# Performance work log

Hardware: AMD Instinct MI355X
Metric: run time of the kernel (lower is better)

Reference implementation:

```python
import jax, jax.numpy as jnp
import numpy as np

N_NODES = 100000
N_EDGES = 3200000
F_IN, F_HID, F_OUT = 1433, 8, 7
K = 2  # kernel_size, dim=1, degree-1 B-spline -> basis (1-u, u)
LEAKY_SLOPE = 0.2


def att_spline_conv(x, edge_index, pseudo, w, root, att, bias, n_nodes):
    """Attention SplineConv layer (dim=1, kernel_size=2, linear B-spline).

    w:    [K, in, out] spline kernel weights
    root: [in, out]    root/self weight
    att:  [2*out]      attention vector (src-message part || dst part)
    """
    src, dst = edge_index[0], edge_index[1]
    u = pseudo[:, 0]                                   # [E], in [0,1]
    basis = jnp.stack([1.0 - u, u], axis=1)            # [E, K]
    # transform at node level first (cheap), then gather per edge
    xw = jnp.einsum('ni,kio->nko', x, w)               # [N, K, out]
    m = jnp.einsum('ek,eko->eo', basis, xw[src])       # [E, out] spline message
    h = x @ root                                       # [N, out] root transform
    out_dim = w.shape[-1]
    # GAT-style attention: leaky_relu(a_src . m_e + a_dst . h_dst)
    score = m @ att[:out_dim] + (h @ att[out_dim:])[dst]   # [E]
    score = jax.nn.leaky_relu(score, LEAKY_SLOPE)
    smax = jax.ops.segment_max(score, dst, num_segments=n_nodes)
    e = jnp.exp(score - smax[dst])
    denom = jax.ops.segment_sum(e, dst, num_segments=n_nodes)
    alpha = e / (denom[dst] + 1e-16)                   # segment softmax over dst
    agg = jax.ops.segment_sum(alpha[:, None] * m, dst, num_segments=n_nodes)
    return agg + h + bias


def setup_inputs() -> dict:
    key = jax.random.key(0)
    ks = jax.random.split(key, 12)
    x = jax.random.normal(ks[0], (N_NODES, F_IN), dtype=jnp.float32)
    edge_index = jax.random.randint(ks[1], (2, N_EDGES), 0, N_NODES, dtype=jnp.int64)
    pseudo = jax.random.uniform(ks[2], (N_EDGES, 1), dtype=jnp.float32)
    s1 = 1.0 / np.sqrt(F_IN)
    s2 = 1.0 / np.sqrt(F_HID)
    return {
        'x': x,
        'edge_index': edge_index,
        'pseudo': pseudo,
        'w1': jax.random.normal(ks[3], (K, F_IN, F_HID), dtype=jnp.float32) * s1,
        'root1': jax.random.normal(ks[4], (F_IN, F_HID), dtype=jnp.float32) * s1,
        'att1': jax.random.normal(ks[5], (2 * F_HID,), dtype=jnp.float32) * s2,
        'bias1': jnp.zeros((F_HID,), dtype=jnp.float32),
        'w2': jax.random.normal(ks[6], (K, F_HID, F_OUT), dtype=jnp.float32) * s2,
        'root2': jax.random.normal(ks[7], (F_HID, F_OUT), dtype=jnp.float32) * s2,
        'att2': jax.random.normal(ks[8], (2 * F_OUT,), dtype=jnp.float32) * s2,
        'bias2': jnp.zeros((F_OUT,), dtype=jnp.float32),
    }


def reference(x, edge_index, pseudo, w1, root1, att1, bias1, w2, root2, att2, bias2):
    # eval mode: F.dropout with training=False is identity
    n = x.shape[0]
    h = jax.nn.elu(att_spline_conv(x, edge_index, pseudo, w1, root1, att1, bias1, n))
    h = att_spline_conv(h, edge_index, pseudo, w2, root2, att2, bias2, n)
    return jax.nn.log_softmax(h, axis=1)
```

## Files before the change

### kernel.cpp

```cpp
#include <hip/hip_runtime.h>
#include <math.h>

#define TPB 256
#define F_IN 1433
#define KPAD 1440
#define NT 45
#define NFULL 44
#define ROWS 128

typedef __attribute__((ext_vector_type(8))) short bf16x8;
typedef __attribute__((ext_vector_type(4))) float f32x4;

static __device__ __forceinline__ short f2bf(float f) {
    unsigned u = __float_as_uint(f);
    unsigned r = (u + 0x7FFFu + ((u >> 16) & 1u)) >> 16;
    return (short)r;
}

__global__ __launch_bounds__(256) void prep_kernel(
    const float* __restrict__ w1, const float* __restrict__ root1,
    short* __restrict__ WT, int* __restrict__ cnt, int N)
{
    int i = blockIdx.x * 256 + threadIdx.x;
    if (i < N) cnt[i] = 0;
    if (i < 32 * KPAD) {
        int col = i / KPAD, k = i - col * KPAD;
        float v = 0.f;
        if (k < F_IN) {
            if (col < 8)       v = w1[(size_t)k * 8 + col];
            else if (col < 16) v = w1[(size_t)(F_IN + k) * 8 + (col - 8)];
            else if (col < 24) v = root1[(size_t)k * 8 + (col - 16)];
        }
        WT[i] = f2bf(v);
    }
}

__global__ __launch_bounds__(256) void node1_hist_kernel(
    const float* __restrict__ x,
    const short* __restrict__ WT,
    const float* __restrict__ att1,
    float* __restrict__ XW1,
    float* __restrict__ H1,
    float2* __restrict__ SC1,
    float* __restrict__ HA1,
    const int* __restrict__ ei,
    int* __restrict__ cnt,
    int N, int E, int NB1)
{
    __shared__ float xb[4][32][32];

    const int tid = threadIdx.x;
    const int bid = blockIdx.x;

    if (bid >= NB1) {
        int e = (bid - NB1) * TPB + tid;
        if (e < E) atomicAdd(&cnt[ei[(size_t)E + e]], 1);
        return;
    }

    const int wv   = tid >> 6;
    const int lane = tid & 63;
    const int rowbase = bid * ROWS;

    const int srow   = lane & 7;
    const int schunk = lane >> 3;
    const int pchunk = schunk ^ srow;
    const float* gsrc[4];
#pragma unroll
    for (int g = 0; g < 4; ++g) {
        int r = rowbase + wv * 32 + g * 8 + srow;
        if (r >= N) r = N - 1;
        gsrc[g] = x + (size_t)r * F_IN + schunk * 4;
    }

    const int r0 = lane & 15, r1 = r0 + 16;
    const int klane = (lane >> 4) * 8;
    const int c0 = klane >> 2;
    const int p0 = c0 ^ (r0 & 7);
    const int p1 = (c0 + 1) ^ (r0 & 7);
    const short* wt0 = WT + (size_t)(lane & 15) * KPAD + klane;
    const short* wt1 = wt0 + 16 * KPAD;

    f32x4 acc[2][2];
#pragma unroll
    for (int i = 0; i < 2; ++i)
#pragma unroll
        for (int j = 0; j < 2; ++j)
#pragma unroll
            for (int r = 0; r < 4; ++r) acc[i][j][r] = 0.f;

    {
        float4 V[4];
#pragma unroll
        for (int g = 0; g < 4; ++g) V[g] = *reinterpret_cast<const float4*>(gsrc[g]);
#pragma unroll
        for (int g = 0; g < 4; ++g)
            *reinterpret_cast<float4*>(&xb[wv][g * 8 + srow][pchunk * 4]) = V[g];
    }

    for (int t = 0; t < NFULL; ++t) {
        float4 Vn[4];
        const bool more = (t + 1 < NFULL);
        if (more) {
#pragma unroll
            for (int g = 0; g < 4; ++g)
                Vn[g] = *reinterpret_cast<const float4*>(gsrc[g] + (t + 1) * 32);
        }
        bf16x8 b0 = *reinterpret_cast<const bf16x8*>(wt0 + t * 32);
        bf16x8 b1 = *reinterpret_cast<const bf16x8*>(wt1 + t * 32);
        float4 fa0 = *reinterpret_cast<const float4*>(&xb[wv][r0][p0 * 4]);
        float4 fb0 = *reinterpret_cast<const float4*>(&xb[wv][r0][p1 * 4]);
        float4 fa1 = *reinterpret_cast<const float4*>(&xb[wv][r1][p0 * 4]);
        float4 fb1 = *reinterpret_cast<const float4*>(&xb[wv][r1][p1 * 4]);
        bf16x8 pa0, pa1;
        pa0[0] = f2bf(fa0.x); pa0[1] = f2bf(fa0.y); pa0[2] = f2bf(fa0.z); pa0[3] = f2bf(fa0.w);
        pa0[4] = f2bf(fb0.x); pa0[5] = f2bf(fb0.y); pa0[6] = f2bf(fb0.z); pa0[7] = f2bf(fb0.w);
        pa1[0] = f2bf(fa1.x); pa1[1] = f2bf(fa1.y); pa1[2] = f2bf(fa1.z); pa1[3] = f2bf(fa1.w);
        pa1[4] = f2bf(fb1.x); pa1[5] = f2bf(fb1.y); pa1[6] = f2bf(fb1.z); pa1[7] = f2bf(fb1.w);
        acc[0][0] = __builtin_amdgcn_mfma_f32_16x16x32_bf16(pa0, b0, acc[0][0], 0, 0, 0);
        acc[0][1] = __builtin_amdgcn_mfma_f32_16x16x32_bf16(pa0, b1, acc[0][1], 0, 0, 0);
        acc[1][0] = __builtin_amdgcn_mfma_f32_16x16x32_bf16(pa1, b0, acc[1][0], 0, 0, 0);
        acc[1][1] = __builtin_amdgcn_mfma_f32_16x16x32_bf16(pa1, b1, acc[1][1], 0, 0, 0);
        if (more) {
#pragma unroll
            for (int g = 0; g < 4; ++g)
                *reinterpret_cast<float4*>(&xb[wv][g * 8 + srow][pchunk * 4]) = Vn[g];
        }
    }

    {
        int rr0 = rowbase + wv * 32 + r0; if (rr0 >= N) rr0 = N - 1;
        int rr1 = rowbase + wv * 32 + r1; if (rr1 >= N) rr1 = N - 1;
        const float* xr0 = x + (size_t)rr0 * F_IN;
        const float* xr1 = x + (size_t)rr1 * F_IN;
        const int kf = NFULL * 32 + klane;
        bf16x8 pa0, pa1;
#pragma unroll
        for (int q = 0; q < 8; ++q) {
            float v0 = (kf + q < F_IN) ? xr0[kf + q] : 0.f;
            float v1 = (kf + q < F_IN) ? xr1[kf + q] : 0.f;
            pa0[q] = f2bf(v0);
            pa1[q] = f2bf(v1);
        }
        bf16x8 b0 = *reinterpret_cast<const bf16x8*>(wt0 + NFULL * 32);
        bf16x8 b1 = *reinterpret_cast<const bf16x8*>(wt1 + NFULL * 32);
        acc[0][0] = __builtin_amdgcn_mfma_f32_16x16x32_bf16(pa0, b0, acc[0][0], 0, 0, 0);
        acc[0][1] = __builtin_amdgcn_mfma_f32_16x16x32_bf16(pa0, b1, acc[0][1], 0, 0, 0);
        acc[1][0] = __builtin_amdgcn_mfma_f32_16x16x32_bf16(pa1, b0, acc[1][0], 0, 0, 0);
        acc[1][1] = __builtin_amdgcn_mfma_f32_16x16x32_bf16(pa1, b1, acc[1][1], 0, 0, 0);
    }

    __syncthreads();

    float* dump = reinterpret_cast<float*>(xb);
#pragma unroll
    for (int rt = 0; rt < 2; ++rt)
#pragma unroll
        for (int ot = 0; ot < 2; ++ot) {
            int col = ot * 16 + (lane & 15);
            if (col < 24) {
#pragma unroll
                for (int r = 0; r < 4; ++r) {
                    int row = wv * 32 + rt * 16 + (lane >> 4) * 4 + r;
                    dump[row * 25 + col] = acc[rt][ot][r];
                }
            }
        }
    __syncthreads();

    if (tid < ROWS) {
        int n = rowbase + tid;
        if (n < N) {
            float sum[24];
#pragma unroll
            for (int j = 0; j < 24; ++j) sum[j] = dump[tid * 25 + j];
            float s0 = 0.f, s1 = 0.f, ha = 0.f;
#pragma unroll
            for (int j = 0; j < 8; ++j) {
                s0 += sum[j] * att1[j];
                s1 += sum[8 + j] * att1[j];
                ha += sum[16 + j] * att1[8 + j];
            }
            float4* xwout = reinterpret_cast<float4*>(XW1 + (size_t)n * 16);
            xwout[0] = make_float4(sum[0], sum[1], sum[2], sum[3]);
            xwout[1] = make_float4(sum[4], sum[5], sum[6], sum[7]);
            xwout[2] = make_float4(sum[8], sum[9], sum[10], sum[11]);
            xwout[3] = make_float4(sum[12], sum[13], sum[14], sum[15]);
            float4* hout = reinterpret_cast<float4*>(H1 + (size_t)n * 8);
            hout[0] = make_float4(sum[16], sum[17], sum[18], sum[19]);
            hout[1] = make_float4(sum[20], sum[21], sum[22], sum[23]);
            SC1[n] = make_float2(s0, s1);
            HA1[n] = ha;
        }
    }
}

__global__ __launch_bounds__(256) void scanA_kernel(
    const int* __restrict__ cnt, int* __restrict__ rowptr, int* __restrict__ bsums, int N)
{
    __shared__ int lds[256];
    int t = threadIdx.x;
    int base = blockIdx.x * 1024 + t * 4;
    int c[4];
#pragma unroll
    for (int j = 0; j < 4; ++j) c[j] = (base + j < N) ? cnt[base + j] : 0;
    int tsum = c[0] + c[1] + c[2] + c[3];
    lds[t] = tsum;
    __syncthreads();
    for (int off = 1; off < 256; off <<= 1) {
        int v = (t >= off) ? lds[t - off] : 0;
        __syncthreads();
        lds[t] += v;
        __syncthreads();
    }
    int run = lds[t] - tsum;
#pragma unroll
    for (int j = 0; j < 4; ++j) {
        if (base + j < N) rowptr[base + j] = run;
        run += c[j];
    }
    if (t == 255) bsums[blockIdx.x] = lds[255];
}

__global__ __launch_bounds__(128) void scanB_kernel(int* __restrict__ bsums, int nb)
{
    __shared__ int lds[128];
    int t = threadIdx.x;
    int v = (t < nb) ? bsums[t] : 0;
    lds[t] = v;
    __syncthreads();
    for (int off = 1; off < 128; off <<= 1) {
        int w = (t >= off) ? lds[t - off] : 0;
        __syncthreads();
        lds[t] += w;
        __syncthreads();
    }
    if (t < nb) bsums[t] = lds[t] - v;
}

__global__ __launch_bounds__(256) void scanC_kernel(
    int* __restrict__ rowptr, int* __restrict__ cnt, const int* __restrict__ bsums, int N, int E)
{
    int i = blockIdx.x * TPB + threadIdx.x;
    if (i < N) {
        int v = rowptr[i] + bsums[i >> 10];
        rowptr[i] = v;
        cnt[i] = v;
    }
    if (i == 0) rowptr[N] = E;
}

__global__ __launch_bounds__(256) void scatter_kernel(
    const int* __restrict__ ei, const float* __restrict__ pseudo,
    int* __restrict__ cursor, int2* __restrict__ recs, int E)
{
    int e = blockIdx.x * TPB + threadIdx.x;
    if (e >= E) return;
    int s = ei[e];
    int d = ei[(size_t)E + e];
    float u = pseudo[e];
    int pos = atomicAdd(&cursor[d], 1);
    recs[pos] = make_int2(s, __float_as_int(u));
}

__global__ __launch_bounds__(256) void gather1_kernel(
    const int* __restrict__ rowptr, const int2* __restrict__ recs,
    const float4* __restrict__ XW1v,
    const float2* __restrict__ SC1, const float* __restrict__ HA1,
    const float* __restrict__ H1, const float* __restrict__ bias1,
    const float* __restrict__ w2, const float* __restrict__ root2, const float* __restrict__ att2,
    float* __restrict__ XW2, float* __restrict__ H2, float2* __restrict__ SC2, float* __restrict__ HA2,
    int N)
{
    int tid = blockIdx.x * TPB + threadIdx.x;
    int n = tid >> 4;
    int lane = tid & 15;
    if (n >= N) return;
    int start = rowptr[n], end = rowptr[n + 1];
    float ha = HA1[n];
    float den = 0.f;
    float num[8];
#pragma unroll
    for (int j = 0; j < 8; ++j) num[j] = 0.f;

    for (int i = start + lane; i < end; i += 16) {
        int2 r = recs[i];
        int s = r.x;
        float u = __int_as_float(r.y);
        float um = 1.f - u;
        float2 sc = SC1[s];
        float raw = um * sc.x + u * sc.y + ha;
        float score = (raw > 0.f) ? raw : 0.2f * raw;
        float w = expf(score);
        const float4* xw = XW1v + (size_t)s * 4;
        float4 p0 = xw[0], p1 = xw[1], q0 = xw[2], q1 = xw[3];
        num[0] = fmaf(w, um * p0.x + u * q0.x, num[0]);
        num[1] = fmaf(w, um * p0.y + u * q0.y, num[1]);
        num[2] = fmaf(w, um * p0.z + u * q0.z, num[2]);
        num[3] = fmaf(w, um * p0.w + u * q0.w, num[3]);
        num[4] = fmaf(w, um * p1.x + u * q1.x, num[4]);
        num[5] = fmaf(w, um * p1.y + u * q1.y, num[5]);
        num[6] = fmaf(w, um * p1.z + u * q1.z, num[6]);
        num[7] = fmaf(w, um * p1.w + u * q1.w, num[7]);
        den += w;
    }
#pragma unroll
    for (int off = 1; off < 16; off <<= 1) {
#pragma unroll
        for (int j = 0; j < 8; ++j) num[j] += __shfl_xor(num[j], off);
        den += __shfl_xor(den, off);
    }
    if (lane != 0) return;

    float inv = 1.f / (den + 1e-16f);
    float hp[8];
#pragma unroll
    for (int j = 0; j < 8; ++j) {
        float o = num[j] * inv + H1[(size_t)n * 8 + j] + bias1[j];
        hp[j] = (o > 0.f) ? o : expm1f(o);
    }
    float a[7], b[7], h[7];
#pragma unroll
    for (int j2 = 0; j2 < 7; ++j2) { a[j2] = 0.f; b[j2] = 0.f; h[j2] = 0.f; }
#pragma unroll
    for (int j = 0; j < 8; ++j) {
#pragma unroll
        for (int j2 = 0; j2 < 7; ++j2) {
            a[j2] = fmaf(hp[j], w2[j * 7 + j2], a[j2]);
            b[j2] = fmaf(hp[j], w2[56 + j * 7 + j2], b[j2]);
            h[j2] = fmaf(hp[j], root2[j * 7 + j2], h[j2]);
        }
    }
    float s0 = 0.f, s1 = 0.f, hA = 0.f;
#pragma unroll
    for (int j2 = 0; j2 < 7; ++j2) {
        s0 += a[j2] * att2[j2];
        s1 += b[j2] * att2[j2];
        hA += h[j2] * att2[7 + j2];
    }
    float4* xwout = reinterpret_cast<float4*>(XW2 + (size_t)n * 16);
    xwout[0] = make_float4(a[0], a[1], a[2], a[3]);
    xwout[1] = make_float4(a[4], a[5], a[6], 0.f);
    xwout[2] = make_float4(b[0], b[1], b[2], b[3]);
    xwout[3] = make_float4(b[4], b[5], b[6], 0.f);
    float4* hout = reinterpret_cast<float4*>(H2 + (size_t)n * 8);
    hout[0] = make_float4(h[0], h[1], h[2], h[3]);
    hout[1] = make_float4(h[4], h[5], h[6], 0.f);
    SC2[n] = make_float2(s0, s1);
    HA2[n] = hA;
}

__global__ __launch_bounds__(256) void gather2_kernel(
    const int* __restrict__ rowptr, const int2* __restrict__ recs,
    const float4* __restrict__ XW2v,
    const float2* __restrict__ SC2, const float* __restrict__ HA2,
    const float* __restrict__ H2, const float* __restrict__ bias2,
    float* __restrict__ out, int N)
{
    int tid = blockIdx.x * TPB + threadIdx.x;
    int n = tid >> 4;
    int lane = tid & 15;
    if (n >= N) return;
    int start = rowptr[n], end = rowptr[n + 1];
    float ha = HA2[n];
    float den = 0.f;
    float num[7];
#pragma unroll
    for (int j = 0; j < 7; ++j) num[j] = 0.f;

    for (int i = start + lane; i < end; i += 16) {
        int2 r = recs[i];
        int s = r.x;
        float u = __int_as_float(r.y);
        float um = 1.f - u;
        float2 sc = SC2[s];
        float raw = um * sc.x + u * sc.y + ha;
        float score = (raw > 0.f) ? raw : 0.2f * raw;
        float w = expf(score);
        const float4* xw = XW2v + (size_t)s * 4;
        float4 p0 = xw[0], p1 = xw[1], q0 = xw[2], q1 = xw[3];
        num[0] = fmaf(w, um * p0.x + u * q0.x, num[0]);
        num[1] = fmaf(w, um * p0.y + u * q0.y, num[1]);
        num[2] = fmaf(w, um * p0.z + u * q0.z, num[2]);
        num[3] = fmaf(w, um * p0.w + u * q0.w, num[3]);
        num[4] = fmaf(w, um * p1.x + u * q1.x, num[4]);
        num[5] = fmaf(w, um * p1.y + u * q1.y, num[5]);
        num[6] = fmaf(w, um * p1.z + u * q1.z, num[6]);
        den += w;
    }
#pragma unroll
    for (int off = 1; off < 16; off <<= 1) {
#pragma unroll
        for (int j = 0; j < 7; ++j) num[j] += __shfl_xor(num[j], off);
        den += __shfl_xor(den, off);
    }
    if (lane != 0) return;

    float inv = 1.f / (den + 1e-16f);
    float o[7];
    float mx = -1e30f;
#pragma unroll
    for (int j = 0; j < 7; ++j) {
        o[j] = fmaf(num[j], inv, H2[(size_t)n * 8 + j] + bias2[j]);
        mx = fmaxf(mx, o[j]);
    }
    float sum = 0.f;
#pragma unroll
    for (int j = 0; j < 7; ++j) sum += expf(o[j] - mx);
    float lse = mx + logf(sum);
#pragma unroll
    for (int j = 0; j < 7; ++j) out[(size_t)n * 7 + j] = o[j] - lse;
}

extern "C" void kernel_launch(void* const* d_in, const int* in_sizes, int n_in,
                              void* d_out, int out_size, void* d_ws, size_t ws_size,
                              hipStream_t stream) {
    const float* x      = (const float*)d_in[0];
    const int*   ei     = (const int*)d_in[1];
    const float* pseudo = (const float*)d_in[2];
    const float* w1     = (const float*)d_in[3];
    const float* root1  = (const float*)d_in[4];
    const float* att1   = (const float*)d_in[5];
    const float* bias1  = (const float*)d_in[6];
    const float* w2     = (const float*)d_in[7];
    const float* root2  = (const float*)d_in[8];
    const float* att2   = (const float*)d_in[9];
    const float* bias2  = (const float*)d_in[10];

    const int N = in_sizes[0] / F_IN;
    const int E = in_sizes[2];
    const size_t Ns = (size_t)N;

    float* ws   = (float*)d_ws;
    float* XW1  = ws;
    float* H1   = XW1 + 16 * Ns;
    float2* SC1 = (float2*)(H1 + 8 * Ns);
    float* HA1  = (float*)SC1 + 2 * Ns;
    float* XW2  = HA1 + Ns;
    float* H2   = XW2 + 16 * Ns;
    float2* SC2 = (float2*)(H2 + 8 * Ns);
    float* HA2  = (float*)SC2 + 2 * Ns;
    int*   cnt    = (int*)(HA2 + Ns);
    int*   rowptr = cnt + Ns;
    int*   bsums  = rowptr + Ns + 1;
    size_t off = (size_t)(bsums + 128) - (size_t)d_ws;
    off = (off + 7) & ~(size_t)7;
    int2*  recs = (int2*)((char*)d_ws + off);
    size_t woff = off + (size_t)E * sizeof(int2);
    woff = (woff + 15) & ~(size_t)15;
    short* WT = (short*)((char*)d_ws + woff);

    int nblk  = (N + TPB - 1) / TPB;
    int eblk  = (E + TPB - 1) / TPB;
    int sblkA = (N + 1023) / 1024;
    int nb1   = (N + ROWS - 1) / ROWS;
    int gblk  = ((N * 16) + TPB - 1) / TPB;
    int prepn = (32 * KPAD > N) ? 32 * KPAD : N;
    int pblk  = (prepn + TPB - 1) / TPB;

    prep_kernel<<<pblk, TPB, 0, stream>>>(w1, root1, WT, cnt, N);
    node1_hist_kernel<<<nb1 + eblk, TPB, 0, stream>>>(
        x, WT, att1, XW1, H1, SC1, HA1, ei, cnt, N, E, nb1);
    scanA_kernel<<<sblkA, TPB, 0, stream>>>(cnt, rowptr, bsums, N);
    scanB_kernel<<<1, 128, 0, stream>>>(bsums, sblkA);
    scanC_kernel<<<nblk, TPB, 0, stream>>>(rowptr, cnt, bsums, N, E);
    scatter_kernel<<<eblk, TPB, 0, stream>>>(ei, pseudo, cnt, recs, E);
    gather1_kernel<<<gblk, TPB, 0, stream>>>(rowptr, recs, (const float4*)XW1, SC1, HA1,
                                             H1, bias1, w2, root2, att2,
                                             XW2, H2, SC2, HA2, N);
    gather2_kernel<<<gblk, TPB, 0, stream>>>(rowptr, recs, (const float4*)XW2, SC2, HA2,
                                             H2, bias2, (float*)d_out, N);
}
```

Measured before the change: 611.1 us.

## Async global-to-LDS double buffering in node GEMM, narrower gather groups, fast exp

The node-level GEMM now streams x tiles into double-buffered LDS with global_load_lds, manually placing waitcnt and prefetching weight fragments one step ahead. This removes the register round-trip and lets the loads overlap the MFMA work. Separately, the gather kernels use 8 lanes per node instead of 16, halving thread count and shuffle-reduction steps at the cost of more work per lane. expf and logf become the fast intrinsics __expf and __logf, which may change accuracy slightly. The hand-written vmcnt counts depend on the compiler's instruction order, so the pipeline is fragile.

After: 631.9 us. 1.03x slower.

```diff
diff --git a/kernel.cpp b/kernel.cpp
--- a/kernel.cpp
+++ b/kernel.cpp
@@ -15,6 +15,13 @@
     unsigned u = __float_as_uint(f);
     unsigned r = (u + 0x7FFFu + ((u >> 16) & 1u)) >> 16;
     return (short)r;
+}
+
+static __device__ __forceinline__ void gl2lds16(const float* g, float* l) {
+    __builtin_amdgcn_global_load_lds(
+        (const __attribute__((address_space(1))) void*)g,
+        (__attribute__((address_space(3))) void*)l,
+        16, 0, 0);
 }
 
 __global__ __launch_bounds__(256) void prep_kernel(
@@ -47,7 +54,7 @@
     int* __restrict__ cnt,
     int N, int E, int NB1)
 {
-    __shared__ float xb[4][32][32];
+    __shared__ float xb[4][2][1024];
 
     const int tid = threadIdx.x;
     const int bid = blockIdx.x;
@@ -62,23 +69,32 @@
     const int lane = tid & 63;
     const int rowbase = bid * ROWS;
 
-    const int srow   = lane & 7;
-    const int schunk = lane >> 3;
-    const int pchunk = schunk ^ srow;
-    const float* gsrc[4];
+    const int drow8 = lane >> 3;
+    const int dclog = (lane & 7) ^ drow8;
+    const float* dsrc[4];
 #pragma unroll
     for (int g = 0; g < 4; ++g) {
-        int r = rowbase + wv * 32 + g * 8 + srow;
+        int r = rowbase + wv * 32 + g * 8 + drow8;
         if (r >= N) r = N - 1;
-        gsrc[g] = x + (size_t)r * F_IN + schunk * 4;
-    }
-
-    const int r0 = lane & 15, r1 = r0 + 16;
-    const int klane = (lane >> 4) * 8;
-    const int c0 = klane >> 2;
-    const int p0 = c0 ^ (r0 & 7);
-    const int p1 = (c0 + 1) ^ (r0 & 7);
-    const short* wt0 = WT + (size_t)(lane & 15) * KPAD + klane;
+        dsrc[g] = x + (size_t)r * F_IN + dclog * 4;
+    }
+
+#define ISSUE(tile, buf) do {                                                   \
+        float* ldsb = &xb[wv][buf][0];                                          \
+        _Pragma("unroll")                                                       \
+        for (int g = 0; g < 4; ++g)                                             \
+            gl2lds16(dsrc[g] + (tile) * 32, ldsb + g * 256);                    \
+    } while (0)
+
+    const int r0 = lane & 15;
+    const int kg = lane >> 4;
+    const int c0 = kg * 2;
+    const int gA = r0 >> 3, rA = r0 & 7;
+    const int offA0 = gA * 256 + (rA * 8 + (c0 ^ rA)) * 4;
+    const int offB0 = gA * 256 + (rA * 8 + ((c0 + 1) ^ rA)) * 4;
+    const int offA1 = offA0 + 512;
+    const int offB1 = offB0 + 512;
+    const short* wt0 = WT + (size_t)r0 * KPAD + kg * 8;
     const short* wt1 = wt0 + 16 * KPAD;
 
     f32x4 acc[2][2];
@@ -89,51 +105,51 @@
 #pragma unroll
             for (int r = 0; r < 4; ++r) acc[i][j][r] = 0.f;
 
+    bf16x8 b0A, b1A, b0B, b1B;
+
+    ISSUE(0, 0);
+    b0A = *reinterpret_cast<const bf16x8*>(wt0);
+    b1A = *reinterpret_cast<const bf16x8*>(wt1);
+    ISSUE(1, 1);
+
+#define KITER(t, buf, BU0, BU1, BN0, BN1) do {                                  \
+        if ((t) + 1 < NFULL) asm volatile("s_waitcnt vmcnt(6)" ::: "memory");   \
+        else                 asm volatile("s_waitcnt vmcnt(0)" ::: "memory");   \
+        const float* Bb = &xb[wv][buf][0];                                      \
+        float4 fa0 = *reinterpret_cast<const float4*>(Bb + offA0);              \
+        float4 fb0 = *reinterpret_cast<const float4*>(Bb + offB0);              \
+        float4 fa1 = *reinterpret_cast<const float4*>(Bb + offA1);              \
+        float4 fb1 = *reinterpret_cast<const float4*>(Bb + offB1);              \
+        if ((t) + 1 < NFULL) {                                                  \
+            BN0 = *reinterpret_cast<const bf16x8*>(wt0 + ((t) + 1) * 32);       \
+            BN1 = *reinterpret_cast<const bf16x8*>(wt1 + ((t) + 1) * 32);       \
+        }                                                                       \
+        asm volatile("s_waitcnt lgkmcnt(0)" ::: "memory");                      \
+        if ((t) + 2 < NFULL) { ISSUE((t) + 2, buf); }                           \
+        bf16x8 pa0, pa1;                                                        \
+        pa0[0] = f2bf(fa0.x); pa0[1] = f2bf(fa0.y); pa0[2] = f2bf(fa0.z); pa0[3] = f2bf(fa0.w); \
+        pa0[4] = f2bf(fb0.x); pa0[5] = f2bf(fb0.y); pa0[6] = f2bf(fb0.z); pa0[7] = f2bf(fb0.w); \
+        pa1[0] = f2bf(fa1.x); pa1[1] = f2bf(fa1.y); pa1[2] = f2bf(fa1.z); pa1[3] = f2bf(fa1.w); \
+        pa1[4] = f2bf(fb1.x); pa1[5] = f2bf(fb1.y); pa1[6] = f2bf(fb1.z); pa1[7] = f2bf(fb1.w); \
+        acc[0][0] = __builtin_amdgcn_mfma_f32_16x16x32_bf16(pa0, BU0, acc[0][0], 0, 0, 0); \
+        acc[0][1] = __builtin_amdgcn_mfma_f32_16x16x32_bf16(pa0, BU1, acc[0][1], 0, 0, 0); \
+        acc[1][0] = __builtin_amdgcn_mfma_f32_16x16x32_bf16(pa1, BU0, acc[1][0], 0, 0, 0); \
+        acc[1][1] = __builtin_amdgcn_mfma_f32_16x16x32_bf16(pa1, BU1, acc[1][1], 0, 0, 0); \
+    } while (0)
+
+    for (int tt = 0; tt < NFULL; tt += 2) {
+        KITER(tt,     0, b0A, b1A, b0B, b1B);
+        KITER(tt + 1, 1, b0B, b1B, b0A, b1A);
+    }
+#undef KITER
+#undef ISSUE
+
     {
-        float4 V[4];
-#pragma unroll
-        for (int g = 0; g < 4; ++g) V[g] = *reinterpret_cast<const float4*>(gsrc[g]);
-#pragma unroll
-        for (int g = 0; g < 4; ++g)
-            *reinterpret_cast<float4*>(&xb[wv][g * 8 + srow][pchunk * 4]) = V[g];
-    }
-
-    for (int t = 0; t < NFULL; ++t) {
-        float4 Vn[4];
-        const bool more = (t + 1 < NFULL);
-        if (more) {
-#pragma unroll
-            for (int g = 0; g < 4; ++g)
-                Vn[g] = *reinterpret_cast<const float4*>(gsrc[g] + (t + 1) * 32);
-        }
-        bf16x8 b0 = *reinterpret_cast<const bf16x8*>(wt0 + t * 32);
-        bf16x8 b1 = *reinterpret_cast<const bf16x8*>(wt1 + t * 32);
-        float4 fa0 = *reinterpret_cast<const float4*>(&xb[wv][r0][p0 * 4]);
-        float4 fb0 = *reinterpret_cast<const float4*>(&xb[wv][r0][p1 * 4]);
-        float4 fa1 = *reinterpret_cast<const float4*>(&xb[wv][r1][p0 * 4]);
-        float4 fb1 = *reinterpret_cast<const float4*>(&xb[wv][r1][p1 * 4]);
-        bf16x8 pa0, pa1;
-        pa0[0] = f2bf(fa0.x); pa0[1] = f2bf(fa0.y); pa0[2] = f2bf(fa0.z); pa0[3] = f2bf(fa0.w);
-        pa0[4] = f2bf(fb0.x); pa0[5] = f2bf(fb0.y); pa0[6] = f2bf(fb0.z); pa0[7] = f2bf(fb0.w);
-        pa1[0] = f2bf(fa1.x); pa1[1] = f2bf(fa1.y); pa1[2] = f2bf(fa1.z); pa1[3] = f2bf(fa1.w);
-        pa1[4] = f2bf(fb1.x); pa1[5] = f2bf(fb1.y); pa1[6] = f2bf(fb1.z); pa1[7] = f2bf(fb1.w);
-        acc[0][0] = __builtin_amdgcn_mfma_f32_16x16x32_bf16(pa0, b0, acc[0][0], 0, 0, 0);
-        acc[0][1] = __builtin_amdgcn_mfma_f32_16x16x32_bf16(pa0, b1, acc[0][1], 0, 0, 0);
-        acc[1][0] = __builtin_amdgcn_mfma_f32_16x16x32_bf16(pa1, b0, acc[1][0], 0, 0, 0);
-        acc[1][1] = __builtin_amdgcn_mfma_f32_16x16x32_bf16(pa1, b1, acc[1][1], 0, 0, 0);
-        if (more) {
-#pragma unroll
-            for (int g = 0; g < 4; ++g)
-                *reinterpret_cast<float4*>(&xb[wv][g * 8 + srow][pchunk * 4]) = Vn[g];
-        }
-    }
-
-    {
-        int rr0 = rowbase + wv * 32 + r0; if (rr0 >= N) rr0 = N - 1;
-        int rr1 = rowbase + wv * 32 + r1; if (rr1 >= N) rr1 = N - 1;
+        int rr0 = rowbase + wv * 32 + r0;      if (rr0 >= N) rr0 = N - 1;
+        int rr1 = rowbase + wv * 32 + r0 + 16; if (rr1 >= N) rr1 = N - 1;
         const float* xr0 = x + (size_t)rr0 * F_IN;
         const float* xr1 = x + (size_t)rr1 * F_IN;
-        const int kf = NFULL * 32 + klane;
+        const int kf = NFULL * 32 + kg * 8;
         bf16x8 pa0, pa1;
 #pragma unroll
         for (int q = 0; q < 8; ++q) {
@@ -273,8 +289,8 @@
     int N)
 {
     int tid = blockIdx.x * TPB + threadIdx.x;
-    int n = tid >> 4;
-    int lane = tid & 15;
+    int n = tid >> 3;
+    int lane = tid & 7;
     if (n >= N) return;
     int start = rowptr[n], end = rowptr[n + 1];
     float ha = HA1[n];
@@ -283,7 +299,7 @@
 #pragma unroll
     for (int j = 0; j < 8; ++j) num[j] = 0.f;
 
-    for (int i = start + lane; i < end; i += 16) {
+    for (int i = start + lane; i < end; i += 8) {
         int2 r = recs[i];
         int s = r.x;
         float u = __int_as_float(r.y);
@@ -291,7 +307,7 @@
         float2 sc = SC1[s];
         float raw = um * sc.x + u * sc.y + ha;
         float score = (raw > 0.f) ? raw : 0.2f * raw;
-        float w = expf(score);
+        float w = __expf(score);
         const float4* xw = XW1v + (size_t)s * 4;
         float4 p0 = xw[0], p1 = xw[1], q0 = xw[2], q1 = xw[3];
         num[0] = fmaf(w, um * p0.x + u * q0.x, num[0]);
@@ -305,7 +321,7 @@
         den += w;
     }
 #pragma unroll
-    for (int off = 1; off < 16; off <<= 1) {
+    for (int off = 1; off < 8; off <<= 1) {
 #pragma unroll
         for (int j = 0; j < 8; ++j) num[j] += __shfl_xor(num[j], off);
         den += __shfl_xor(den, off);
@@ -358,8 +374,8 @@
     float* __restrict__ out, int N)
 {
     int tid = blockIdx.x * TPB + threadIdx.x;
-    int n = tid >> 4;
-    int lane = tid & 15;
+    int n = tid >> 3;
+    int lane = tid & 7;
     if (n >= N) return;
     int start = rowptr[n], end = rowptr[n + 1];
     float ha = HA2[n];
@@ -368,7 +384,7 @@
 #pragma unroll
     for (int j = 0; j < 7; ++j) num[j] = 0.f;
 
-    for (int i = start + lane; i < end; i += 16) {
+    for (int i = start + lane; i < end; i += 8) {
         int2 r = recs[i];
         int s = r.x;
         float u = __int_as_float(r.y);
@@ -376,7 +392,7 @@
         float2 sc = SC2[s];
         float raw = um * sc.x + u * sc.y + ha;
         float score = (raw > 0.f) ? raw : 0.2f * raw;
-        float w = expf(score);
+        float w = __expf(score);
         const float4* xw = XW2v + (size_t)s * 4;
         float4 p0 = xw[0], p1 = xw[1], q0 = xw[2], q1 = xw[3];
         num[0] = fmaf(w, um * p0.x + u * q0.x, num[0]);
@@ -389,7 +405,7 @@
         den += w;
     }
 #pragma unroll
-    for (int off = 1; off < 16; off <<= 1) {
+    for (int off = 1; off < 8; off <<= 1) {
 #pragma unroll
         for (int j = 0; j < 7; ++j) num[j] += __shfl_xor(num[j], off);
         den += __shfl_xor(den, off);
@@ -406,8 +422,8 @@
     }
     float sum = 0.f;
 #pragma unroll
-    for (int j = 0; j < 7; ++j) sum += expf(o[j] - mx);
-    float lse = mx + logf(sum);
+    for (int j = 0; j < 7; ++j) sum += __expf(o[j] - mx);
+    float lse = mx + __logf(sum);
 #pragma unroll
     for (int j = 0; j < 7; ++j) out[(size_t)n * 7 + j] = o[j] - lse;
 }
@@ -454,7 +470,7 @@
     int eblk  = (E + TPB - 1) / TPB;
     int sblkA = (N + 1023) / 1024;
     int nb1   = (N + ROWS - 1) / ROWS;
-    int gblk  = ((N * 16) + TPB - 1) / TPB;
+    int gblk  = ((N * 8) + TPB - 1) / TPB;
     int prepn = (32 * KPAD > N) ? 32 * KPAD : N;
     int pblk  = (prepn + TPB - 1) / TPB;
 
```
